# Performance work log

Hardware: AMD Instinct MI355X
Metric: run time of the kernel (lower is better)

The kernel has to match this reference:

```python
import jax, jax.numpy as jnp
import numpy as np

HISTORY = 128  # self-inclusive causal window width

def _layernorm(x, g, b, eps=1e-5):
    mu = jnp.mean(x, axis=-1, keepdims=True)
    var = jnp.var(x, axis=-1, keepdims=True)
    return (x - mu) * jax.lax.rsqrt(var + eps) * g + b

def setup_inputs() -> dict:
    key = jax.random.key(0)
    ks = jax.random.split(key, 8)
    dim, hid, B, T = 64, 256, 4, 4096
    s = lambda fan_in: 1.0 / np.sqrt(fan_in)
    return {
        "x": jax.random.normal(ks[0], (B, T, dim), jnp.float32),
        "W_in": jax.random.normal(ks[1], (dim, hid), jnp.float32) * s(dim),
        "b_in": jnp.zeros((hid,), jnp.float32),
        "W_qkv": jax.random.normal(ks[2], (hid, 3 * hid), jnp.float32) * s(hid),
        "b_qkv": jnp.zeros((3 * hid,), jnp.float32),
        "g_attn": jnp.ones((hid,), jnp.float32),
        "be_attn": jnp.zeros((hid,), jnp.float32),
        "g_mlp": jnp.ones((hid,), jnp.float32),
        "be_mlp": jnp.zeros((hid,), jnp.float32),
        "W1": jax.random.normal(ks[3], (hid, hid), jnp.float32) * s(hid),
        "b1": jnp.zeros((hid,), jnp.float32),
        "W2": jax.random.normal(ks[4], (hid, hid), jnp.float32) * s(hid),
        "b2": jnp.zeros((hid,), jnp.float32),
        "W_out": jax.random.normal(ks[5], (hid, dim), jnp.float32) * s(hid),
        "b_out": jnp.zeros((dim,), jnp.float32),
    }

def reference(x, W_in, b_in, W_qkv, b_qkv, g_attn, be_attn, g_mlp, be_mlp,
              W1, b1, W2, b2, W_out, b_out):
    B, T, _ = x.shape
    hid = W_in.shape[1]
    h = x @ W_in + b_in                                  # (B,T,hid)
    qkv = _layernorm(h, g_attn, be_attn) @ W_qkv + b_qkv
    q, k, v = jnp.split(qkv, 3, axis=-1)
    scale = 1.0 / jnp.sqrt(jnp.asarray(hid, x.dtype))
    scores = jnp.einsum('bqd,bkd->bqk', q, k) * scale    # (B,T,T)
    idx = jnp.arange(T)
    delta = idx[:, None] - idx[None, :]
    mask = (delta >= 0) & (delta <= HISTORY)             # self-inclusive window
    scores = jnp.where(mask[None], scores, jnp.finfo(x.dtype).min)
    attn = jax.nn.softmax(scores, axis=-1)
    attn_out = jnp.einsum('bqk,bkd->bqd', attn, v)
    h = h + attn_out                                     # residual (dropout=0)
    m = _layernorm(h, g_mlp, be_mlp)
    m = jax.nn.gelu(m @ W1 + b1, approximate=False) @ W2 + b2
    h = h + m
    return h @ W_out + b_out                             # (B,T,dim)
```

## Files before the change

kernel.cpp:

```cpp
#include <hip/hip_runtime.h>
#include <hip/hip_bf16.h>
#include <math.h>

typedef short bf8 __attribute__((ext_vector_type(8)));
typedef float f4  __attribute__((ext_vector_type(4)));

#define DEV static __device__ __forceinline__

DEV f4 MFMA(bf8 a, bf8 b, f4 c) { return __builtin_amdgcn_mfma_f32_16x16x32_bf16(a, b, c, 0, 0, 0); }

DEV unsigned short f2bf(float f) {
  union { float f; unsigned int u; } v; v.f = f;
  unsigned int r = v.u + 0x7FFFu + ((v.u >> 16) & 1u);
  return (unsigned short)(r >> 16);
}
DEV float bf2f(unsigned short u) {
  union { unsigned int u; float f; } v; v.u = ((unsigned int)u) << 16;
  return v.f;
}

struct P15 { const void* p[15]; };

DEV float ldin(const void* p, int i, bool bf) {
  return bf ? bf2f(((const unsigned short*)p)[i]) : ((const float*)p)[i];
}

#define PB_IN 0
#define PB_QKV 256
#define PB1 1024
#define PB2 1280
#define PB_OUT 1536
#define PGA 1600
#define PBA 1856
#define PGM 2112
#define PBM 2368

__global__ __launch_bounds__(256) void k_prep(P15 in,
    unsigned short* __restrict__ WinT, unsigned short* __restrict__ WqkvT,
    unsigned short* __restrict__ W1T, unsigned short* __restrict__ W2T,
    unsigned short* __restrict__ WoutT, float* __restrict__ par)
{
  const bool bf = (*(const unsigned int*)in.p[5]) == 0x3F803F80u;
  const int E0 = 16384;
  const int E1 = E0 + 196608;
  const int E2 = E1 + 65536;
  const int E3 = E2 + 65536;
  const int E4 = E3 + 16384;
  const int E5 = E4 + 2624;
  for (int i = blockIdx.x * 256 + threadIdx.x; i < E5; i += gridDim.x * 256) {
    if (i < E0) {
      int k = i >> 8, n = i & 255;
      WinT[n * 64 + k] = f2bf(ldin(in.p[1], i, bf));
    } else if (i < E1) {
      int j = i - E0, k = j / 768, n = j - k * 768;
      WqkvT[n * 256 + k] = f2bf(ldin(in.p[3], j, bf));
    } else if (i < E2) {
      int j = i - E1, k = j >> 8, n = j & 255;
      W1T[n * 256 + k] = f2bf(ldin(in.p[9], j, bf));
    } else if (i < E3) {
      int j = i - E2, k = j >> 8, n = j & 255;
      W2T[n * 256 + k] = f2bf(ldin(in.p[11], j, bf));
    } else if (i < E4) {
      int j = i - E3, k = j >> 6, n = j & 63;
      WoutT[n * 256 + k] = f2bf(ldin(in.p[13], j, bf));
    } else {
      int j = i - E4;
      const void* src; int o;
      if (j < 256)       { src = in.p[2];  o = j; }
      else if (j < 1024) { src = in.p[4];  o = j - 256; }
      else if (j < 1280) { src = in.p[10]; o = j - 1024; }
      else if (j < 1536) { src = in.p[12]; o = j - 1280; }
      else if (j < 1600) { src = in.p[14]; o = j - 1536; }
      else if (j < 1856) { src = in.p[5];  o = j - 1600; }
      else if (j < 2112) { src = in.p[6];  o = j - 1856; }
      else if (j < 2368) { src = in.p[7];  o = j - 2112; }
      else               { src = in.p[8];  o = j - 2368; }
      par[j] = ldin(src, o, bf);
    }
  }
}

__global__ __launch_bounds__(512, 4) void k_in_qkv(const void* __restrict__ xin,
    const unsigned short* __restrict__ WinT, const unsigned short* __restrict__ WqkvT,
    const float* __restrict__ par, const void* __restrict__ probe,
    float* __restrict__ h, unsigned short* __restrict__ qb,
    unsigned short* __restrict__ kb, unsigned short* __restrict__ vT)
{
  __shared__ unsigned short smem[35328];
  __shared__ float sStat[8][16][2];
  unsigned short* sX   = smem;
  unsigned short* sW   = smem + 4608;
  unsigned short* sLn1 = smem;
  unsigned short* sV   = smem + 16896;
  const int tid = threadIdx.x, lane = tid & 63, w = tid >> 6;
  const int l15 = lane & 15, l4 = lane >> 4;
  const int m0 = blockIdx.x * 64;
  const int bb = m0 >> 12, q0 = m0 & 4095;
  const bool bf = (*(const unsigned int*)probe) == 0x3F803F80u;
  const f4 z = {0.f, 0.f, 0.f, 0.f};

  {
    int r = tid >> 3, c8 = (tid & 7) * 8;
    if (bf) {
      *(bf8*)&sX[r * 72 + c8] = *(const bf8*)((const unsigned short*)xin + (m0 + r) * 64 + c8);
    } else {
      const float* xf = (const float*)xin + (m0 + r) * 64 + c8;
      float4 f0 = *(const float4*)xf, f1 = *(const float4*)(xf + 4);
      unsigned short t8[8] = { f2bf(f0.x), f2bf(f0.y), f2bf(f0.z), f2bf(f0.w),
                               f2bf(f1.x), f2bf(f1.y), f2bf(f1.z), f2bf(f1.w) };
      *(bf8*)&sX[r * 72 + c8] = *(const bf8*)t8;
    }
  }
  for (int t = tid; t < 2048; t += 512) {
    int r = t >> 3, c8 = (t & 7) * 8;
    *(bf8*)&sW[r * 72 + c8] = *(const bf8*)&WinT[r * 64 + c8];
  }
  __syncthreads();

  const int rm = w & 3, cg = w >> 2;
  f4 acc1[8];
  #pragma unroll
  for (int f = 0; f < 8; ++f) acc1[f] = z;
  {
    bf8 ax0 = *(const bf8*)&sX[(16 * rm + l15) * 72 + l4 * 8];
    bf8 ax1 = *(const bf8*)&sX[(16 * rm + l15) * 72 + 32 + l4 * 8];
    #pragma unroll
    for (int f = 0; f < 8; ++f) {
      bf8 b0 = *(const bf8*)&sW[(128 * cg + 16 * f + l15) * 72 + l4 * 8];
      bf8 b1 = *(const bf8*)&sW[(128 * cg + 16 * f + l15) * 72 + 32 + l4 * 8];
      acc1[f] = MFMA(ax0, b0, acc1[f]);
      acc1[f] = MFMA(ax1, b1, acc1[f]);
    }
  }
  {
    float s[4] = {0,0,0,0}, s2[4] = {0,0,0,0};
    #pragma unroll
    for (int f = 0; f < 8; ++f) {
      float bias = par[PB_IN + 128 * cg + 16 * f + l15];
      #pragma unroll
      for (int r = 0; r < 4; ++r) {
        float v = acc1[f][r] + bias; acc1[f][r] = v;
        s[r] += v; s2[r] += v * v;
      }
    }
    #pragma unroll
    for (int m = 1; m <= 8; m <<= 1) {
      #pragma unroll
      for (int r = 0; r < 4; ++r) { s[r] += __shfl_xor(s[r], m); s2[r] += __shfl_xor(s2[r], m); }
    }
    if (l15 == 0) {
      #pragma unroll
      for (int r = 0; r < 4; ++r) { sStat[w][4 * l4 + r][0] = s[r]; sStat[w][4 * l4 + r][1] = s2[r]; }
    }
    __syncthreads();
    float mu[4], rstd[4];
    #pragma unroll
    for (int r = 0; r < 4; ++r) {
      float st  = s[r]  + sStat[w ^ 4][4 * l4 + r][0];
      float st2 = s2[r] + sStat[w ^ 4][4 * l4 + r][1];
      mu[r] = st * (1.f / 256.f);
      rstd[r] = rsqrtf(st2 * (1.f / 256.f) - mu[r] * mu[r] + 1e-5f);
    }
    #pragma unroll
    for (int f = 0; f < 8; ++f) {
      int col = 128 * cg + 16 * f + l15;
      float g = par[PGA + col], be = par[PBA + col];
      #pragma unroll
      for (int r = 0; r < 4; ++r) {
        int rl = 16 * rm + 4 * l4 + r;
        h[(m0 + rl) * 256 + col] = acc1[f][r];
        sLn1[rl * 264 + col] = f2bf((acc1[f][r] - mu[r]) * rstd[r] * g + be);
      }
    }
  }
  __syncthreads();

  const int cw = 96 * w;
  #pragma unroll
  for (int p = 0; p < 2; ++p) {
    f4 acc[4][3];
    #pragma unroll
    for (int rt = 0; rt < 4; ++rt)
      #pragma unroll
      for (int f = 0; f < 3; ++f) acc[rt][f] = z;
    #pragma unroll
    for (int ks = 0; ks < 8; ++ks) {
      bf8 a0 = *(const bf8*)&sLn1[(l15) * 264 + ks * 32 + l4 * 8];
      bf8 a1 = *(const bf8*)&sLn1[(16 + l15) * 264 + ks * 32 + l4 * 8];
      bf8 a2 = *(const bf8*)&sLn1[(32 + l15) * 264 + ks * 32 + l4 * 8];
      bf8 a3 = *(const bf8*)&sLn1[(48 + l15) * 264 + ks * 32 + l4 * 8];
      #pragma unroll
      for (int f = 0; f < 3; ++f) {
        bf8 b = *(const bf8*)&WqkvT[(cw + 48 * p + 16 * f + l15) * 256 + ks * 32 + l4 * 8];
        acc[0][f] = MFMA(a0, b, acc[0][f]);
        acc[1][f] = MFMA(a1, b, acc[1][f]);
        acc[2][f] = MFMA(a2, b, acc[2][f]);
        acc[3][f] = MFMA(a3, b, acc[3][f]);
      }
    }
    #pragma unroll
    for (int f = 0; f < 3; ++f) {
      int col = cw + 48 * p + 16 * f + l15;
      float bias = par[PB_QKV + col];
      #pragma unroll
      for (int rt = 0; rt < 4; ++rt) {
        #pragma unroll
        for (int r = 0; r < 4; ++r) {
          int row = 16 * rt + 4 * l4 + r;
          unsigned short bv = f2bf(acc[rt][f][r] + bias);
          if (col < 256)      qb[(m0 + row) * 256 + col] = bv;
          else if (col < 512) kb[(m0 + row) * 256 + (col - 256)] = bv;
          else                sV[(col - 512) * 72 + row] = bv;
        }
      }
    }
  }
  __syncthreads();
  for (int ch = tid; ch < 2048; ch += 512) {
    int d = ch >> 3, c8 = (ch & 7) * 8;
    *(bf8*)&vT[(bb * 256 + d) * 4096 + q0 + c8] = *(const bf8*)&sV[d * 72 + c8];
  }
}

__global__ __launch_bounds__(512, 4) void k_attn_mlp(const unsigned short* __restrict__ qb,
    const unsigned short* __restrict__ kb, const unsigned short* __restrict__ vT,
    const float* __restrict__ h, const unsigned short* __restrict__ W1T,
    const unsigned short* __restrict__ W2T, const unsigned short* __restrict__ WoutT,
    const float* __restrict__ par, void* __restrict__ dout, const void* __restrict__ probe)
{
  __shared__ unsigned short smem[35328];
  __shared__ float sStat[8][16][2];
  unsigned short* sKs  = smem;
  unsigned short* sVs  = smem;
  unsigned short* sLn2 = smem;
  unsigned short* sM   = smem;
  unsigned short* sP   = smem + 18432;
  unsigned short* sH3  = smem + 18432;
  const int tid = threadIdx.x, lane = tid & 63, w = tid >> 6;
  const int l15 = lane & 15, l4 = lane >> 4;
  const int m0 = blockIdx.x * 64;
  const int bb = m0 >> 12, q0 = m0 & 4095, kstart = q0 - 128;
  const bool bf = (*(const unsigned int*)probe) == 0x3F803F80u;
  const f4 z = {0.f, 0.f, 0.f, 0.f};
  const int wq = w & 3, wc = w >> 2;

  bf8 qreg[8];
  #pragma unroll
  for (int ks = 0; ks < 8; ++ks)
    qreg[ks] = *(const bf8*)&qb[(m0 + 16 * wq + l15) * 256 + ks * 32 + l4 * 8];

  f4 sacc[6];
  #pragma unroll
  for (int i = 0; i < 6; ++i) sacc[i] = z;
  #pragma unroll
  for (int c = 0; c < 3; ++c) {
    for (int t = tid; t < 2048; t += 512) {
      int r = t >> 5, c8 = (t & 31) * 8;
      int j = kstart + 64 * c + r; if (j < 0) j = 0;
      *(bf8*)&sKs[r * 264 + c8] = *(const bf8*)&kb[(bb * 4096 + j) * 256 + c8];
    }
    __syncthreads();
    #pragma unroll
    for (int ks = 0; ks < 8; ++ks) {
      #pragma unroll
      for (int j2 = 0; j2 < 2; ++j2) {
        bf8 bk = *(const bf8*)&sKs[(32 * wc + 16 * j2 + l15) * 264 + ks * 32 + l4 * 8];
        sacc[2 * c + j2] = MFMA(qreg[ks], bk, sacc[2 * c + j2]);
      }
    }
    __syncthreads();
  }

  float inv[4];
  {
    const float scale = 0.0625f;
    float mx[4] = {-1e30f, -1e30f, -1e30f, -1e30f};
    #pragma unroll
    for (int c = 0; c < 3; ++c) {
      #pragma unroll
      for (int j2 = 0; j2 < 2; ++j2) {
        int kk = 64 * c + 32 * wc + 16 * j2 + l15;
        #pragma unroll
        for (int r = 0; r < 4; ++r) {
          int qi = 16 * wq + 4 * l4 + r;
          bool valid = (kk >= qi) && (kk <= qi + 128) && (kstart + kk >= 0);
          float sv = valid ? sacc[2 * c + j2][r] * scale : -1e30f;
          sacc[2 * c + j2][r] = sv;
          mx[r] = fmaxf(mx[r], sv);
        }
      }
    }
    #pragma unroll
    for (int m = 1; m <= 8; m <<= 1) {
      #pragma unroll
      for (int r = 0; r < 4; ++r) mx[r] = fmaxf(mx[r], __shfl_xor(mx[r], m));
    }
    if (l15 == 0) {
      #pragma unroll
      for (int r = 0; r < 4; ++r) sStat[w][4 * l4 + r][0] = mx[r];
    }
    __syncthreads();
    #pragma unroll
    for (int r = 0; r < 4; ++r) mx[r] = fmaxf(mx[r], sStat[w ^ 4][4 * l4 + r][0]);
    float sum[4] = {0,0,0,0};
    #pragma unroll
    for (int c = 0; c < 3; ++c) {
      #pragma unroll
      for (int j2 = 0; j2 < 2; ++j2) {
        #pragma unroll
        for (int r = 0; r < 4; ++r) {
          float p = __expf(sacc[2 * c + j2][r] - mx[r]);
          sacc[2 * c + j2][r] = p;
          sum[r] += p;
        }
      }
    }
    #pragma unroll
    for (int m = 1; m <= 8; m <<= 1) {
      #pragma unroll
      for (int r = 0; r < 4; ++r) sum[r] += __shfl_xor(sum[r], m);
    }
    if (l15 == 0) {
      #pragma unroll
      for (int r = 0; r < 4; ++r) sStat[w][4 * l4 + r][1] = sum[r];
    }
    __syncthreads();
    #pragma unroll
    for (int r = 0; r < 4; ++r) inv[r] = 1.f / (sum[r] + sStat[w ^ 4][4 * l4 + r][1]);
    #pragma unroll
    for (int c = 0; c < 3; ++c) {
      #pragma unroll
      for (int j2 = 0; j2 < 2; ++j2) {
        int kk = 64 * c + 32 * wc + 16 * j2 + l15;
        #pragma unroll
        for (int r = 0; r < 4; ++r)
          sP[(16 * wq + 4 * l4 + r) * 200 + kk] = f2bf(sacc[2 * c + j2][r]);
      }
    }
  }

  f4 oacc[8];
  #pragma unroll
  for (int f = 0; f < 8; ++f) oacc[f] = z;
  #pragma unroll
  for (int c = 0; c < 3; ++c) {
    __syncthreads();
    for (int t = tid; t < 2048; t += 512) {
      int d = t >> 3, c8 = (t & 7) * 8;
      int j0 = kstart + 64 * c + c8; if (j0 < 0) j0 = 0;
      *(bf8*)&sVs[d * 72 + c8] = *(const bf8*)&vT[(bb * 256 + d) * 4096 + j0];
    }
    __syncthreads();
    #pragma unroll
    for (int ks = 0; ks < 2; ++ks) {
      bf8 a = *(const bf8*)&sP[(16 * wq + l15) * 200 + 64 * c + ks * 32 + l4 * 8];
      #pragma unroll
      for (int f = 0; f < 8; ++f) {
        bf8 bv = *(const bf8*)&sVs[(128 * wc + 16 * f + l15) * 72 + ks * 32 + l4 * 8];
        oacc[f] = MFMA(a, bv, oacc[f]);
      }
    }
  }
  __syncthreads();

  {
    float s[4] = {0,0,0,0}, s2[4] = {0,0,0,0};
    #pragma unroll
    for (int f = 0; f < 8; ++f) {
      #pragma unroll
      for (int r = 0; r < 4; ++r) {
        float v = h[(m0 + 16 * wq + 4 * l4 + r) * 256 + 128 * wc + 16 * f + l15]
                  + oacc[f][r] * inv[r];
        oacc[f][r] = v; s[r] += v; s2[r] += v * v;
      }
    }
    #pragma unroll
    for (int m = 1; m <= 8; m <<= 1) {
      #pragma unroll
      for (int r = 0; r < 4; ++r) { s[r] += __shfl_xor(s[r], m); s2[r] += __shfl_xor(s2[r], m); }
    }
    if (l15 == 0) {
      #pragma unroll
      for (int r = 0; r < 4; ++r) { sStat[w][4 * l4 + r][0] = s[r]; sStat[w][4 * l4 + r][1] = s2[r]; }
    }
    __syncthreads();
    float mu[4], rstd[4];
    #pragma unroll
    for (int r = 0; r < 4; ++r) {
      float st  = s[r]  + sStat[w ^ 4][4 * l4 + r][0];
      float st2 = s2[r] + sStat[w ^ 4][4 * l4 + r][1];
      mu[r] = st * (1.f / 256.f);
      rstd[r] = rsqrtf(st2 * (1.f / 256.f) - mu[r] * mu[r] + 1e-5f);
    }
    #pragma unroll
    for (int f = 0; f < 8; ++f) {
      int col = 128 * wc + 16 * f + l15;
      float g = par[PGM + col], be = par[PBM + col];
      #pragma unroll
      for (int r = 0; r < 4; ++r)
        sLn2[(16 * wq + 4 * l4 + r) * 264 + col] = f2bf((oacc[f][r] - mu[r]) * rstd[r] * g + be);
    }
  }
  __syncthreads();

  {
    bf8 aA[8];
    #pragma unroll
    for (int ks = 0; ks < 8; ++ks)
      aA[ks] = *(const bf8*)&sLn2[(16 * wq + l15) * 264 + ks * 32 + l4 * 8];
    __syncthreads();
    #pragma unroll
    for (int f = 0; f < 8; ++f) {
      f4 ac = z;
      const unsigned short* bp = &W1T[(128 * wc + 16 * f + l15) * 256 + l4 * 8];
      #pragma unroll
      for (int ks = 0; ks < 8; ++ks) {
        bf8 b = *(const bf8*)&bp[ks * 32];
        ac = MFMA(aA[ks], b, ac);
      }
      int col = 128 * wc + 16 * f + l15;
      float bias = par[PB1 + col];
      #pragma unroll
      for (int r = 0; r < 4; ++r) {
        float v = ac[r] + bias;
        sM[(16 * wq + 4 * l4 + r) * 264 + col] =
            f2bf(0.5f * v * (1.0f + erff(v * 0.70710678118654752f)));
      }
    }
  }
  __syncthreads();

  {
    bf8 aM[8];
    #pragma unroll
    for (int ks = 0; ks < 8; ++ks)
      aM[ks] = *(const bf8*)&sM[(16 * wq + l15) * 264 + ks * 32 + l4 * 8];
    #pragma unroll
    for (int f = 0; f < 8; ++f) {
      f4 ac = z;
      const unsigned short* bp = &W2T[(128 * wc + 16 * f + l15) * 256 + l4 * 8];
      #pragma unroll
      for (int ks = 0; ks < 8; ++ks) {
        bf8 b = *(const bf8*)&bp[ks * 32];
        ac = MFMA(aM[ks], b, ac);
      }
      int col = 128 * wc + 16 * f + l15;
      float bias = par[PB2 + col];
      #pragma unroll
      for (int r = 0; r < 4; ++r)
        sH3[(16 * wq + 4 * l4 + r) * 264 + col] = f2bf(oacc[f][r] + ac[r] + bias);
    }
  }
  __syncthreads();

  {
    bf8 aO[8];
    #pragma unroll
    for (int ks = 0; ks < 8; ++ks)
      aO[ks] = *(const bf8*)&sH3[(16 * wq + l15) * 264 + ks * 32 + l4 * 8];
    #pragma unroll
    for (int j = 0; j < 2; ++j) {
      f4 ac = z;
      const unsigned short* bp = &WoutT[(32 * wc + 16 * j + l15) * 256 + l4 * 8];
      #pragma unroll
      for (int ks = 0; ks < 8; ++ks) {
        bf8 b = *(const bf8*)&bp[ks * 32];
        ac = MFMA(aO[ks], b, ac);
      }
      int col = 32 * wc + 16 * j + l15;
      float bias = par[PB_OUT + col];
      #pragma unroll
      for (int r = 0; r < 4; ++r) {
        int row = m0 + 16 * wq + 4 * l4 + r;
        float v = ac[r] + bias;
        if (bf) ((unsigned short*)dout)[row * 64 + col] = f2bf(v);
        else    ((float*)dout)[row * 64 + col] = v;
      }
    }
  }
}

extern "C" void kernel_launch(void* const* d_in, const int* in_sizes, int n_in,
                              void* d_out, int out_size, void* d_ws, size_t ws_size,
                              hipStream_t stream)
{
  (void)in_sizes; (void)n_in; (void)out_size; (void)ws_size;
  char* ws = (char*)d_ws;
  size_t off = 0;
  auto A = [&](size_t bytes) { void* p = (void*)(ws + off); off += (bytes + 255) & ~(size_t)255; return p; };

  unsigned short* WinT  = (unsigned short*)A(32768);
  unsigned short* WqkvT = (unsigned short*)A(393216);
  unsigned short* W1T   = (unsigned short*)A(131072);
  unsigned short* W2T   = (unsigned short*)A(131072);
  unsigned short* WoutT = (unsigned short*)A(32768);
  float* par            = (float*)A(10496);
  float* h              = (float*)A(16777216);
  unsigned short* qb    = (unsigned short*)A(8388608);
  unsigned short* kb    = (unsigned short*)A(8388608);
  unsigned short* vT    = (unsigned short*)A(8388608);

  P15 in;
  for (int i = 0; i < 15; ++i) in.p[i] = d_in[i];

  k_prep    <<<dim3(512), dim3(256), 0, stream>>>(in, WinT, WqkvT, W1T, W2T, WoutT, par);
  k_in_qkv  <<<dim3(256), dim3(512), 0, stream>>>(d_in[0], WinT, WqkvT, par, d_in[5], h, qb, kb, vT);
  k_attn_mlp<<<dim3(256), dim3(512), 0, stream>>>(qb, kb, vT, h, W1T, W2T, WoutT, par, d_out, d_in[5]);
}
```

Before: 178.6 us.

## Halve row tile to 32, double grid, store residual h as bf16

Both main kernels now handle 32 rows per block instead of 64, so the grid grows from 256 to 512 blocks. Warps are regrouped into 2 row groups by 4 column groups, with four-way cross-warp reductions for the layernorm and softmax statistics. Shared-memory footprints shrink, and one redundant barrier in the PV loop is dropped. The residual h buffer is stored as bf16 instead of fp32, which halves that traffic but loses residual precision; each block also re-fetches the full weight and key/value window for fewer rows.

```diff
diff --git a/kernel.cpp b/kernel.cpp
--- a/kernel.cpp
+++ b/kernel.cpp
@@ -83,23 +83,23 @@
 __global__ __launch_bounds__(512, 4) void k_in_qkv(const void* __restrict__ xin,
     const unsigned short* __restrict__ WinT, const unsigned short* __restrict__ WqkvT,
     const float* __restrict__ par, const void* __restrict__ probe,
-    float* __restrict__ h, unsigned short* __restrict__ qb,
+    unsigned short* __restrict__ hb, unsigned short* __restrict__ qb,
     unsigned short* __restrict__ kb, unsigned short* __restrict__ vT)
 {
-  __shared__ unsigned short smem[35328];
+  __shared__ unsigned short smem[20736];
   __shared__ float sStat[8][16][2];
   unsigned short* sX   = smem;
-  unsigned short* sW   = smem + 4608;
+  unsigned short* sW   = smem + 2304;
   unsigned short* sLn1 = smem;
-  unsigned short* sV   = smem + 16896;
+  unsigned short* sV   = smem + 8448;
   const int tid = threadIdx.x, lane = tid & 63, w = tid >> 6;
   const int l15 = lane & 15, l4 = lane >> 4;
-  const int m0 = blockIdx.x * 64;
+  const int m0 = blockIdx.x * 32;
   const int bb = m0 >> 12, q0 = m0 & 4095;
   const bool bf = (*(const unsigned int*)probe) == 0x3F803F80u;
   const f4 z = {0.f, 0.f, 0.f, 0.f};
 
-  {
+  if (tid < 256) {
     int r = tid >> 3, c8 = (tid & 7) * 8;
     if (bf) {
       *(bf8*)&sX[r * 72 + c8] = *(const bf8*)((const unsigned short*)xin + (m0 + r) * 64 + c8);
@@ -117,17 +117,17 @@
   }
   __syncthreads();
 
-  const int rm = w & 3, cg = w >> 2;
-  f4 acc1[8];
-  #pragma unroll
-  for (int f = 0; f < 8; ++f) acc1[f] = z;
-  {
-    bf8 ax0 = *(const bf8*)&sX[(16 * rm + l15) * 72 + l4 * 8];
-    bf8 ax1 = *(const bf8*)&sX[(16 * rm + l15) * 72 + 32 + l4 * 8];
-    #pragma unroll
-    for (int f = 0; f < 8; ++f) {
-      bf8 b0 = *(const bf8*)&sW[(128 * cg + 16 * f + l15) * 72 + l4 * 8];
-      bf8 b1 = *(const bf8*)&sW[(128 * cg + 16 * f + l15) * 72 + 32 + l4 * 8];
+  const int wq = w & 1, cg = w >> 1;
+  f4 acc1[4];
+  #pragma unroll
+  for (int f = 0; f < 4; ++f) acc1[f] = z;
+  {
+    bf8 ax0 = *(const bf8*)&sX[(16 * wq + l15) * 72 + l4 * 8];
+    bf8 ax1 = *(const bf8*)&sX[(16 * wq + l15) * 72 + 32 + l4 * 8];
+    #pragma unroll
+    for (int f = 0; f < 4; ++f) {
+      bf8 b0 = *(const bf8*)&sW[(64 * cg + 16 * f + l15) * 72 + l4 * 8];
+      bf8 b1 = *(const bf8*)&sW[(64 * cg + 16 * f + l15) * 72 + 32 + l4 * 8];
       acc1[f] = MFMA(ax0, b0, acc1[f]);
       acc1[f] = MFMA(ax1, b1, acc1[f]);
     }
@@ -135,8 +135,8 @@
   {
     float s[4] = {0,0,0,0}, s2[4] = {0,0,0,0};
     #pragma unroll
-    for (int f = 0; f < 8; ++f) {
-      float bias = par[PB_IN + 128 * cg + 16 * f + l15];
+    for (int f = 0; f < 4; ++f) {
+      float bias = par[PB_IN + 64 * cg + 16 * f + l15];
       #pragma unroll
       for (int r = 0; r < 4; ++r) {
         float v = acc1[f][r] + bias; acc1[f][r] = v;
@@ -156,19 +156,23 @@
     float mu[4], rstd[4];
     #pragma unroll
     for (int r = 0; r < 4; ++r) {
-      float st  = s[r]  + sStat[w ^ 4][4 * l4 + r][0];
-      float st2 = s2[r] + sStat[w ^ 4][4 * l4 + r][1];
+      float st = 0.f, st2 = 0.f;
+      #pragma unroll
+      for (int p = 0; p < 4; ++p) {
+        st  += sStat[wq + 2 * p][4 * l4 + r][0];
+        st2 += sStat[wq + 2 * p][4 * l4 + r][1];
+      }
       mu[r] = st * (1.f / 256.f);
       rstd[r] = rsqrtf(st2 * (1.f / 256.f) - mu[r] * mu[r] + 1e-5f);
     }
     #pragma unroll
-    for (int f = 0; f < 8; ++f) {
-      int col = 128 * cg + 16 * f + l15;
+    for (int f = 0; f < 4; ++f) {
+      int col = 64 * cg + 16 * f + l15;
       float g = par[PGA + col], be = par[PBA + col];
       #pragma unroll
       for (int r = 0; r < 4; ++r) {
-        int rl = 16 * rm + 4 * l4 + r;
-        h[(m0 + rl) * 256 + col] = acc1[f][r];
+        int rl = 16 * wq + 4 * l4 + r;
+        hb[(m0 + rl) * 256 + col] = f2bf(acc1[f][r]);
         sLn1[rl * 264 + col] = f2bf((acc1[f][r] - mu[r]) * rstd[r] * g + be);
       }
     }
@@ -176,59 +180,52 @@
   __syncthreads();
 
   const int cw = 96 * w;
-  #pragma unroll
-  for (int p = 0; p < 2; ++p) {
-    f4 acc[4][3];
-    #pragma unroll
-    for (int rt = 0; rt < 4; ++rt)
-      #pragma unroll
-      for (int f = 0; f < 3; ++f) acc[rt][f] = z;
-    #pragma unroll
-    for (int ks = 0; ks < 8; ++ks) {
-      bf8 a0 = *(const bf8*)&sLn1[(l15) * 264 + ks * 32 + l4 * 8];
-      bf8 a1 = *(const bf8*)&sLn1[(16 + l15) * 264 + ks * 32 + l4 * 8];
-      bf8 a2 = *(const bf8*)&sLn1[(32 + l15) * 264 + ks * 32 + l4 * 8];
-      bf8 a3 = *(const bf8*)&sLn1[(48 + l15) * 264 + ks * 32 + l4 * 8];
-      #pragma unroll
-      for (int f = 0; f < 3; ++f) {
-        bf8 b = *(const bf8*)&WqkvT[(cw + 48 * p + 16 * f + l15) * 256 + ks * 32 + l4 * 8];
-        acc[0][f] = MFMA(a0, b, acc[0][f]);
-        acc[1][f] = MFMA(a1, b, acc[1][f]);
-        acc[2][f] = MFMA(a2, b, acc[2][f]);
-        acc[3][f] = MFMA(a3, b, acc[3][f]);
-      }
-    }
-    #pragma unroll
-    for (int f = 0; f < 3; ++f) {
-      int col = cw + 48 * p + 16 * f + l15;
-      float bias = par[PB_QKV + col];
-      #pragma unroll
-      for (int rt = 0; rt < 4; ++rt) {
-        #pragma unroll
-        for (int r = 0; r < 4; ++r) {
-          int row = 16 * rt + 4 * l4 + r;
-          unsigned short bv = f2bf(acc[rt][f][r] + bias);
-          if (col < 256)      qb[(m0 + row) * 256 + col] = bv;
-          else if (col < 512) kb[(m0 + row) * 256 + (col - 256)] = bv;
-          else                sV[(col - 512) * 72 + row] = bv;
-        }
+  f4 acc[2][6];
+  #pragma unroll
+  for (int rt = 0; rt < 2; ++rt)
+    #pragma unroll
+    for (int f = 0; f < 6; ++f) acc[rt][f] = z;
+  #pragma unroll
+  for (int ks = 0; ks < 8; ++ks) {
+    bf8 a0 = *(const bf8*)&sLn1[(l15) * 264 + ks * 32 + l4 * 8];
+    bf8 a1 = *(const bf8*)&sLn1[(16 + l15) * 264 + ks * 32 + l4 * 8];
+    #pragma unroll
+    for (int f = 0; f < 6; ++f) {
+      bf8 b = *(const bf8*)&WqkvT[(cw + 16 * f + l15) * 256 + ks * 32 + l4 * 8];
+      acc[0][f] = MFMA(a0, b, acc[0][f]);
+      acc[1][f] = MFMA(a1, b, acc[1][f]);
+    }
+  }
+  #pragma unroll
+  for (int f = 0; f < 6; ++f) {
+    int col = cw + 16 * f + l15;
+    float bias = par[PB_QKV + col];
+    #pragma unroll
+    for (int rt = 0; rt < 2; ++rt) {
+      #pragma unroll
+      for (int r = 0; r < 4; ++r) {
+        int row = 16 * rt + 4 * l4 + r;
+        unsigned short bv = f2bf(acc[rt][f][r] + bias);
+        if (col < 256)      qb[(m0 + row) * 256 + col] = bv;
+        else if (col < 512) kb[(m0 + row) * 256 + (col - 256)] = bv;
+        else                sV[(col - 512) * 40 + row] = bv;
       }
     }
   }
   __syncthreads();
-  for (int ch = tid; ch < 2048; ch += 512) {
-    int d = ch >> 3, c8 = (ch & 7) * 8;
-    *(bf8*)&vT[(bb * 256 + d) * 4096 + q0 + c8] = *(const bf8*)&sV[d * 72 + c8];
+  for (int ch = tid; ch < 1024; ch += 512) {
+    int d = ch >> 2, c8 = (ch & 3) * 8;
+    *(bf8*)&vT[(bb * 256 + d) * 4096 + q0 + c8] = *(const bf8*)&sV[d * 40 + c8];
   }
 }
 
 __global__ __launch_bounds__(512, 4) void k_attn_mlp(const unsigned short* __restrict__ qb,
     const unsigned short* __restrict__ kb, const unsigned short* __restrict__ vT,
-    const float* __restrict__ h, const unsigned short* __restrict__ W1T,
+    const unsigned short* __restrict__ hb, const unsigned short* __restrict__ W1T,
     const unsigned short* __restrict__ W2T, const unsigned short* __restrict__ WoutT,
     const float* __restrict__ par, void* __restrict__ dout, const void* __restrict__ probe)
 {
-  __shared__ unsigned short smem[35328];
+  __shared__ unsigned short smem[26880];
   __shared__ float sStat[8][16][2];
   unsigned short* sKs  = smem;
   unsigned short* sVs  = smem;
@@ -238,20 +235,20 @@
   unsigned short* sH3  = smem + 18432;
   const int tid = threadIdx.x, lane = tid & 63, w = tid >> 6;
   const int l15 = lane & 15, l4 = lane >> 4;
-  const int m0 = blockIdx.x * 64;
+  const int m0 = blockIdx.x * 32;
   const int bb = m0 >> 12, q0 = m0 & 4095, kstart = q0 - 128;
   const bool bf = (*(const unsigned int*)probe) == 0x3F803F80u;
   const f4 z = {0.f, 0.f, 0.f, 0.f};
-  const int wq = w & 3, wc = w >> 2;
+  const int wq = w & 1, wc = w >> 1;
 
   bf8 qreg[8];
   #pragma unroll
   for (int ks = 0; ks < 8; ++ks)
     qreg[ks] = *(const bf8*)&qb[(m0 + 16 * wq + l15) * 256 + ks * 32 + l4 * 8];
 
-  f4 sacc[6];
-  #pragma unroll
-  for (int i = 0; i < 6; ++i) sacc[i] = z;
+  f4 sacc[3];
+  #pragma unroll
+  for (int i = 0; i < 3; ++i) sacc[i] = z;
   #pragma unroll
   for (int c = 0; c < 3; ++c) {
     for (int t = tid; t < 2048; t += 512) {
@@ -262,11 +259,8 @@
     __syncthreads();
     #pragma unroll
     for (int ks = 0; ks < 8; ++ks) {
-      #pragma unroll
-      for (int j2 = 0; j2 < 2; ++j2) {
-        bf8 bk = *(const bf8*)&sKs[(32 * wc + 16 * j2 + l15) * 264 + ks * 32 + l4 * 8];
-        sacc[2 * c + j2] = MFMA(qreg[ks], bk, sacc[2 * c + j2]);
-      }
+      bf8 bk = *(const bf8*)&sKs[(16 * wc + l15) * 264 + ks * 32 + l4 * 8];
+      sacc[c] = MFMA(qreg[ks], bk, sacc[c]);
     }
     __syncthreads();
   }
@@ -277,17 +271,14 @@
     float mx[4] = {-1e30f, -1e30f, -1e30f, -1e30f};
     #pragma unroll
     for (int c = 0; c < 3; ++c) {
-      #pragma unroll
-      for (int j2 = 0; j2 < 2; ++j2) {
-        int kk = 64 * c + 32 * wc + 16 * j2 + l15;
-        #pragma unroll
-        for (int r = 0; r < 4; ++r) {
-          int qi = 16 * wq + 4 * l4 + r;
-          bool valid = (kk >= qi) && (kk <= qi + 128) && (kstart + kk >= 0);
-          float sv = valid ? sacc[2 * c + j2][r] * scale : -1e30f;
-          sacc[2 * c + j2][r] = sv;
-          mx[r] = fmaxf(mx[r], sv);
-        }
+      int kk = 64 * c + 16 * wc + l15;
+      #pragma unroll
+      for (int r = 0; r < 4; ++r) {
+        int qi = 16 * wq + 4 * l4 + r;
+        bool valid = (kk >= qi) && (kk <= qi + 128) && (kstart + kk >= 0);
+        float sv = valid ? sacc[c][r] * scale : -1e30f;
+        sacc[c][r] = sv;
+        mx[r] = fmaxf(mx[r], sv);
       }
     }
     #pragma unroll
@@ -301,18 +292,20 @@
     }
     __syncthreads();
     #pragma unroll
-    for (int r = 0; r < 4; ++r) mx[r] = fmaxf(mx[r], sStat[w ^ 4][4 * l4 + r][0]);
+    for (int r = 0; r < 4; ++r) {
+      float m2 = -1e30f;
+      #pragma unroll
+      for (int p = 0; p < 4; ++p) m2 = fmaxf(m2, sStat[wq + 2 * p][4 * l4 + r][0]);
+      mx[r] = m2;
+    }
     float sum[4] = {0,0,0,0};
     #pragma unroll
     for (int c = 0; c < 3; ++c) {
       #pragma unroll
-      for (int j2 = 0; j2 < 2; ++j2) {
-        #pragma unroll
-        for (int r = 0; r < 4; ++r) {
-          float p = __expf(sacc[2 * c + j2][r] - mx[r]);
-          sacc[2 * c + j2][r] = p;
-          sum[r] += p;
-        }
+      for (int r = 0; r < 4; ++r) {
+        float p = __expf(sacc[c][r] - mx[r]);
+        sacc[c][r] = p;
+        sum[r] += p;
       }
     }
     #pragma unroll
@@ -326,25 +319,26 @@
     }
     __syncthreads();
     #pragma unroll
-    for (int r = 0; r < 4; ++r) inv[r] = 1.f / (sum[r] + sStat[w ^ 4][4 * l4 + r][1]);
+    for (int r = 0; r < 4; ++r) {
+      float st = 0.f;
+      #pragma unroll
+      for (int p = 0; p < 4; ++p) st += sStat[wq + 2 * p][4 * l4 + r][1];
+      inv[r] = 1.f / st;
+    }
     #pragma unroll
     for (int c = 0; c < 3; ++c) {
-      #pragma unroll
-      for (int j2 = 0; j2 < 2; ++j2) {
-        int kk = 64 * c + 32 * wc + 16 * j2 + l15;
-        #pragma unroll
-        for (int r = 0; r < 4; ++r)
-          sP[(16 * wq + 4 * l4 + r) * 200 + kk] = f2bf(sacc[2 * c + j2][r]);
-      }
-    }
-  }
-
-  f4 oacc[8];
-  #pragma unroll
-  for (int f = 0; f < 8; ++f) oacc[f] = z;
+      int kk = 64 * c + 16 * wc + l15;
+      #pragma unroll
+      for (int r = 0; r < 4; ++r)
+        sP[(16 * wq + 4 * l4 + r) * 200 + kk] = f2bf(sacc[c][r]);
+    }
+  }
+
+  f4 oacc[4];
+  #pragma unroll
+  for (int f = 0; f < 4; ++f) oacc[f] = z;
   #pragma unroll
   for (int c = 0; c < 3; ++c) {
-    __syncthreads();
     for (int t = tid; t < 2048; t += 512) {
       int d = t >> 3, c8 = (t & 7) * 8;
       int j0 = kstart + 64 * c + c8; if (j0 < 0) j0 = 0;
@@ -355,21 +349,21 @@
     for (int ks = 0; ks < 2; ++ks) {
       bf8 a = *(const bf8*)&sP[(16 * wq + l15) * 200 + 64 * c + ks * 32 + l4 * 8];
       #pragma unroll
-      for (int f = 0; f < 8; ++f) {
-        bf8 bv = *(const bf8*)&sVs[(128 * wc + 16 * f + l15) * 72 + ks * 32 + l4 * 8];
+      for (int f = 0; f < 4; ++f) {
+        bf8 bv = *(const bf8*)&sVs[(64 * wc + 16 * f + l15) * 72 + ks * 32 + l4 * 8];
         oacc[f] = MFMA(a, bv, oacc[f]);
       }
     }
-  }
-  __syncthreads();
+    if (c < 2) __syncthreads();
+  }
 
   {
     float s[4] = {0,0,0,0}, s2[4] = {0,0,0,0};
     #pragma unroll
-    for (int f = 0; f < 8; ++f) {
-      #pragma unroll
-      for (int r = 0; r < 4; ++r) {
-        float v = h[(m0 + 16 * wq + 4 * l4 + r) * 256 + 128 * wc + 16 * f + l15]
+    for (int f = 0; f < 4; ++f) {
+      #pragma unroll
+      for (int r = 0; r < 4; ++r) {
+        float v = bf2f(hb[(m0 + 16 * wq + 4 * l4 + r) * 256 + 64 * wc + 16 * f + l15])
                   + oacc[f][r] * inv[r];
         oacc[f][r] = v; s[r] += v; s2[r] += v * v;
       }
@@ -387,14 +381,18 @@
     float mu[4], rstd[4];
     #pragma unroll
     for (int r = 0; r < 4; ++r) {
-      float st  = s[r]  + sStat[w ^ 4][4 * l4 + r][0];
-      float st2 = s2[r] + sStat[w ^ 4][4 * l4 + r][1];
+      float st = 0.f, st2 = 0.f;
+      #pragma unroll
+      for (int p = 0; p < 4; ++p) {
+        st  += sStat[wq + 2 * p][4 * l4 + r][0];
+        st2 += sStat[wq + 2 * p][4 * l4 + r][1];
+      }
       mu[r] = st * (1.f / 256.f);
       rstd[r] = rsqrtf(st2 * (1.f / 256.f) - mu[r] * mu[r] + 1e-5f);
     }
     #pragma unroll
-    for (int f = 0; f < 8; ++f) {
-      int col = 128 * wc + 16 * f + l15;
+    for (int f = 0; f < 4; ++f) {
+      int col = 64 * wc + 16 * f + l15;
       float g = par[PGM + col], be = par[PBM + col];
       #pragma unroll
       for (int r = 0; r < 4; ++r)
@@ -410,15 +408,15 @@
       aA[ks] = *(const bf8*)&sLn2[(16 * wq + l15) * 264 + ks * 32 + l4 * 8];
     __syncthreads();
     #pragma unroll
-    for (int f = 0; f < 8; ++f) {
+    for (int f = 0; f < 4; ++f) {
       f4 ac = z;
-      const unsigned short* bp = &W1T[(128 * wc + 16 * f + l15) * 256 + l4 * 8];
+      const unsigned short* bp = &W1T[(64 * wc + 16 * f + l15) * 256 + l4 * 8];
       #pragma unroll
       for (int ks = 0; ks < 8; ++ks) {
         bf8 b = *(const bf8*)&bp[ks * 32];
         ac = MFMA(aA[ks], b, ac);
       }
-      int col = 128 * wc + 16 * f + l15;
+      int col = 64 * wc + 16 * f + l15;
       float bias = par[PB1 + col];
       #pragma unroll
       for (int r = 0; r < 4; ++r) {
@@ -436,15 +434,15 @@
     for (int ks = 0; ks < 8; ++ks)
       aM[ks] = *(const bf8*)&sM[(16 * wq + l15) * 264 + ks * 32 + l4 * 8];
     #pragma unroll
-    for (int f = 0; f < 8; ++f) {
+    for (int f = 0; f < 4; ++f) {
       f4 ac = z;
-      const unsigned short* bp = &W2T[(128 * wc + 16 * f + l15) * 256 + l4 * 8];
+      const unsigned short* bp = &W2T[(64 * wc + 16 * f + l15) * 256 + l4 * 8];
       #pragma unroll
       for (int ks = 0; ks < 8; ++ks) {
         bf8 b = *(const bf8*)&bp[ks * 32];
         ac = MFMA(aM[ks], b, ac);
       }
-      int col = 128 * wc + 16 * f + l15;
+      int col = 64 * wc + 16 * f + l15;
       float bias = par[PB2 + col];
       #pragma unroll
       for (int r = 0; r < 4; ++r)
@@ -458,24 +456,21 @@
     #pragma unroll
     for (int ks = 0; ks < 8; ++ks)
       aO[ks] = *(const bf8*)&sH3[(16 * wq + l15) * 264 + ks * 32 + l4 * 8];
-    #pragma unroll
-    for (int j = 0; j < 2; ++j) {
-      f4 ac = z;
-      const unsigned short* bp = &WoutT[(32 * wc + 16 * j + l15) * 256 + l4 * 8];
-      #pragma unroll
-      for (int ks = 0; ks < 8; ++ks) {
-        bf8 b = *(const bf8*)&bp[ks * 32];
-        ac = MFMA(aO[ks], b, ac);
-      }
-      int col = 32 * wc + 16 * j + l15;
-      float bias = par[PB_OUT + col];
-      #pragma unroll
-      for (int r = 0; r < 4; ++r) {
-        int row = m0 + 16 * wq + 4 * l4 + r;
-        float v = ac[r] + bias;
-        if (bf) ((unsigned short*)dout)[row * 64 + col] = f2bf(v);
-        else    ((float*)dout)[row * 64 + col] = v;
-      }
+    f4 ac = z;
+    const unsigned short* bp = &WoutT[(16 * wc + l15) * 256 + l4 * 8];
+    #pragma unroll
+    for (int ks = 0; ks < 8; ++ks) {
+      bf8 b = *(const bf8*)&bp[ks * 32];
+      ac = MFMA(aO[ks], b, ac);
+    }
+    int col = 16 * wc + l15;
+    float bias = par[PB_OUT + col];
+    #pragma unroll
+    for (int r = 0; r < 4; ++r) {
+      int row = m0 + 16 * wq + 4 * l4 + r;
+      float v = ac[r] + bias;
+      if (bf) ((unsigned short*)dout)[row * 64 + col] = f2bf(v);
+      else    ((float*)dout)[row * 64 + col] = v;
     }
   }
 }
@@ -495,7 +490,7 @@
   unsigned short* W2T   = (unsigned short*)A(131072);
   unsigned short* WoutT = (unsigned short*)A(32768);
   float* par            = (float*)A(10496);
-  float* h              = (float*)A(16777216);
+  unsigned short* hb    = (unsigned short*)A(8388608);
   unsigned short* qb    = (unsigned short*)A(8388608);
   unsigned short* kb    = (unsigned short*)A(8388608);
   unsigned short* vT    = (unsigned short*)A(8388608);
@@ -504,6 +499,6 @@
   for (int i = 0; i < 15; ++i) in.p[i] = d_in[i];
 
   k_prep    <<<dim3(512), dim3(256), 0, stream>>>(in, WinT, WqkvT, W1T, W2T, WoutT, par);
-  k_in_qkv  <<<dim3(256), dim3(512), 0, stream>>>(d_in[0], WinT, WqkvT, par, d_in[5], h, qb, kb, vT);
-  k_attn_mlp<<<dim3(256), dim3(512), 0, stream>>>(qb, kb, vT, h, W1T, W2T, WoutT, par, d_out, d_in[5]);
-}
+  k_in_qkv  <<<dim3(512), dim3(512), 0, stream>>>(d_in[0], WinT, WqkvT, par, d_in[5], hb, qb, kb, vT);
+  k_attn_mlp<<<dim3(512), dim3(512), 0, stream>>>(qb, kb, vT, hb, W1T, W2T, WoutT, par, d_out, d_in[5]);
+}
```

Result: no change. 179.3 us (+0.4%).
